# Kernel tuning notes

Measured on AMD Instinct MI355X. Metric: run time of the kernel, lower is better.

## Reference

```python
import jax, jax.numpy as jnp
import numpy as np

B, D, E = 8192, 2048, 8


def setup_inputs() -> dict:
    key = jax.random.key(0)
    k1, k2, k3, k4 = jax.random.split(key, 4)
    x = jax.random.normal(k1, (B, D), dtype=jnp.float32)
    W = jax.random.normal(k2, (E, D, D), dtype=jnp.float32) * (1.0 / np.sqrt(D))
    b = jax.random.normal(k3, (E, D), dtype=jnp.float32) * 0.02
    module_indices = jax.random.randint(k4, (B,), 0, E, dtype=jnp.int64)
    return {"x": x, "W": W, "b": b, "module_indices": module_indices}


def reference(x, W, b, module_indices):
    # Each row i of x is processed by expert module_indices[i]:
    #   out[i] = x[i] @ W[e] + b[e],  e = module_indices[i]
    # Vectorized as: run every expert on every token (E dense GEMMs),
    # then select the assigned expert per token via one-hot combine.
    y_all = jnp.einsum('bd,edo->beo', x, W) + b[None, :, :]   # [B, E, D]
    onehot = jax.nn.one_hot(module_indices, W.shape[0], dtype=x.dtype)  # [B, E]
    out = jnp.einsum('beo,be->bo', y_all, onehot)             # [B, D]
    return out
```

## Files before the change

### kernel.cpp

```cpp
#include <hip/hip_runtime.h>
#include <hip/hip_bf16.h>
#include <stdint.h>


#define B_TOK 8192
#define DIM   2048
#define NEXP  8
#define BM 128
#define BN 128
#define BK 32

typedef __attribute__((ext_vector_type(4))) float f32x4;
typedef __attribute__((ext_vector_type(8))) short s16x8;

__device__ __forceinline__ uint32_t f2bf(float f) {
    uint32_t u = __float_as_uint(f);
    uint32_t r = u + 0x7fffu + ((u >> 16) & 1u);
    return r >> 16;
}

__device__ __forceinline__ void async16(const void* g, void* l) {
    __builtin_amdgcn_global_load_lds(
        (const __attribute__((address_space(1))) uint32_t*)g,
        (__attribute__((address_space(3))) uint32_t*)l, 16, 0, 0);
}

__global__ __launch_bounds__(256) void k_route(const int* __restrict__ idx,
                                               int* __restrict__ meta,
                                               int* __restrict__ perm) {
    __shared__ int cnt[256][9];
    __shared__ int offS[NEXP + 1];
    int t = threadIdx.x;
    int myIdx[32];
    #pragma unroll
    for (int i = 0; i < 32; ++i) myIdx[i] = idx[t * 32 + i];
    int c[NEXP] = {0, 0, 0, 0, 0, 0, 0, 0};
    #pragma unroll
    for (int i = 0; i < 32; ++i) {
        int e = myIdx[i];
        #pragma unroll
        for (int k = 0; k < NEXP; ++k) c[k] += (e == k) ? 1 : 0;
    }
    #pragma unroll
    for (int k = 0; k < NEXP; ++k) cnt[t][k] = c[k];
    __syncthreads();
    if (t < NEXP) {
        int run = 0;
        for (int j = 0; j < 256; ++j) { int v = cnt[j][t]; cnt[j][t] = run; run += v; }
        offS[t] = run;
    }
    __syncthreads();
    if (t == 0) {
        int off = 0;
        #pragma unroll
        for (int e = 0; e < NEXP; ++e) {
            int v = offS[e];
            offS[e] = off; meta[16 + e] = off; off += v;
        }
        offS[NEXP] = off; meta[16 + NEXP] = off;
    }
    __syncthreads();
    int base[NEXP];
    #pragma unroll
    for (int k = 0; k < NEXP; ++k) base[k] = offS[k] + cnt[t][k];
    #pragma unroll
    for (int i = 0; i < 32; ++i) {
        int e = myIdx[i];
        int pos = 0;
        #pragma unroll
        for (int k = 0; k < NEXP; ++k) pos += (e == k) ? base[k] : 0;
        perm[pos] = t * 32 + i;
        #pragma unroll
        for (int k = 0; k < NEXP; ++k) base[k] += (e == k) ? 1 : 0;
    }
}

__global__ __launch_bounds__(256) void k_gather(const float* __restrict__ x,
                                                const int* __restrict__ perm,
                                                uint16_t* __restrict__ xs) {
    int p = blockIdx.x;
    int src = perm[p];
    int t = threadIdx.x;
    const float4* xin = (const float4*)(x + (size_t)src * DIM);
    float4 a = xin[2 * t];
    float4 c = xin[2 * t + 1];
    uint4 o;
    o.x = f2bf(a.x) | (f2bf(a.y) << 16);
    o.y = f2bf(a.z) | (f2bf(a.w) << 16);
    o.z = f2bf(c.x) | (f2bf(c.y) << 16);
    o.w = f2bf(c.z) | (f2bf(c.w) << 16);
    *(uint4*)(xs + (size_t)p * DIM + t * 8) = o;
}

__global__ __launch_bounds__(256) void k_wt(const float* __restrict__ W,
                                            uint16_t* __restrict__ Wt) {
    __shared__ uint32_t lds[64][65];
    int e = blockIdx.z, d0 = blockIdx.x * 128, o0 = blockIdx.y * 64;
    int t = threadIdx.x;
    const float* Wp = W + ((size_t)e * DIM + d0) * DIM + o0;
    #pragma unroll
    for (int p = 0; p < 4; ++p) {
        int dp = p * 16 + (t >> 4);
        int oc = (t & 15) * 4;
        const float* r0 = Wp + (size_t)(2 * dp) * DIM + oc;
        float4 v0 = *(const float4*)r0;
        float4 v1 = *(const float4*)(r0 + DIM);
        uint32_t w0 = f2bf(v0.x) | (f2bf(v1.x) << 16);
        uint32_t w1 = f2bf(v0.y) | (f2bf(v1.y) << 16);
        uint32_t w2 = f2bf(v0.z) | (f2bf(v1.z) << 16);
        uint32_t w3 = f2bf(v0.w) | (f2bf(v1.w) << 16);
        lds[oc + 0][dp ^ (((oc + 0) & 15) << 2)] = w0;
        lds[oc + 1][dp ^ (((oc + 1) & 15) << 2)] = w1;
        lds[oc + 2][dp ^ (((oc + 2) & 15) << 2)] = w2;
        lds[oc + 3][dp ^ (((oc + 3) & 15) << 2)] = w3;
    }
    __syncthreads();
    uint16_t* Wo = Wt + ((size_t)e * DIM + o0) * DIM + d0;
    #pragma unroll
    for (int q = 0; q < 4; ++q) {
        int o = q * 16 + (t >> 4);
        int cb = ((t & 15) * 4) ^ ((o & 15) << 2);
        uint4 w = *(const uint4*)&lds[o][cb];
        *(uint4*)(Wo + (size_t)o * DIM + (t & 15) * 8) = w;
    }
}

__global__ __launch_bounds__(256) void k_gemm(
    const uint16_t* __restrict__ xs, const uint16_t* __restrict__ Wt,
    const float* __restrict__ bias, const int* __restrict__ meta,
    const int* __restrict__ perm, float* __restrict__ out) {
    __shared__ uint16_t As[BM * BK];
    __shared__ uint16_t Bs[BN * BK];
    __shared__ int permS[BM];

    int id = blockIdx.y;
    int e = -1, seg0 = 0, segc = 0;
    for (int i = 0; i < NEXP; ++i) {
        int o0 = meta[16 + i], o1 = meta[16 + i + 1];
        int tiles = (o1 - o0 + BM - 1) / BM;
        if (id < tiles) { e = i; seg0 = o0; segc = o1 - o0; break; }
        id -= tiles;
    }
    if (e < 0) return;
    int m0 = seg0 + id * BM;
    int valid = segc - id * BM; if (valid > BM) valid = BM;
    int n0 = blockIdx.x * BN;

    int tid = threadIdx.x;
    if (tid < BM) permS[tid] = (tid < valid) ? perm[m0 + tid] : 0;

    int wave = tid >> 6, lane = tid & 63;
    int wm = (wave >> 1) * 64, wn = (wave & 1) * 64;
    int lr = lane & 15, quad = lane >> 4;

    f32x4 acc[4][4] = {};

    const uint16_t* aG = xs + (size_t)m0 * DIM;
    const uint16_t* bG = Wt + ((size_t)e * DIM + n0) * DIM;

    for (int k0 = 0; k0 < DIM; k0 += BK) {
        #pragma unroll
        for (int ro = 0; ro < 2; ++ro) {
            int ch = ro * 256 + tid;
            int row = ch >> 2, kc = (ch & 3) * 8;
            async16(aG + (size_t)row * DIM + k0 + kc, As + ch * 8);
            async16(bG + (size_t)row * DIM + k0 + kc, Bs + ch * 8);
        }
        __syncthreads();

        s16x8 af[4], bf[4];
        #pragma unroll
        for (int i = 0; i < 4; ++i)
            af[i] = *(const s16x8*)(As + (wm + i * 16 + lr) * BK + quad * 8);
        #pragma unroll
        for (int i = 0; i < 4; ++i)
            bf[i] = *(const s16x8*)(Bs + (wn + i * 16 + lr) * BK + quad * 8);
        #pragma unroll
        for (int i = 0; i < 4; ++i)
            #pragma unroll
            for (int j = 0; j < 4; ++j)
                acc[i][j] = __builtin_amdgcn_mfma_f32_16x16x32_bf16(af[i], bf[j], acc[i][j], 0, 0, 0);
        __syncthreads();
    }

    #pragma unroll
    for (int j = 0; j < 4; ++j) {
        int col = n0 + wn + j * 16 + lr;
        float bv = bias[e * DIM + col];
        #pragma unroll
        for (int i = 0; i < 4; ++i) {
            #pragma unroll
            for (int r = 0; r < 4; ++r) {
                int lrow = wm + i * 16 + quad * 4 + r;
                if (lrow < valid) {
                    out[(size_t)permS[lrow] * DIM + col] = acc[i][j][r] + bv;
                }
            }
        }
    }
}

extern "C" void kernel_launch(void* const* d_in, const int* in_sizes, int n_in,
                              void* d_out, int out_size, void* d_ws, size_t ws_size,
                              hipStream_t stream) {
    const float* x    = (const float*)d_in[0];
    const float* W    = (const float*)d_in[1];
    const float* bias = (const float*)d_in[2];
    const int*   idx  = (const int*)d_in[3];
    float* out = (float*)d_out;

    char* ws = (char*)d_ws;
    int* meta = (int*)ws;
    int* perm = (int*)(ws + 256);
    uint16_t* xs = (uint16_t*)(ws + 65536);
    uint16_t* Wt = (uint16_t*)(ws + 65536 + (size_t)(B_TOK + BM) * DIM * 2);

    k_route<<<1, 256, 0, stream>>>(idx, meta, perm);
    k_gather<<<B_TOK, 256, 0, stream>>>(x, perm, xs);
    k_wt<<<dim3(DIM / 128, DIM / 64, NEXP), 256, 0, stream>>>(W, Wt);
    k_gemm<<<dim3(DIM / BN, B_TOK / BM + NEXP, 1), 256, 0, stream>>>(
        xs, Wt, bias, meta, perm, out);
}
```

Before: 412.5 us.

## Enlarge GEMM tiles, double-buffer swizzled LDS, fuse prep kernels and gather

Merges routing, x-to-bf16 conversion and W transpose into a single prep launch, and moves the token gather into the GEMM's load addressing via perm. The GEMM uses 256x256x64 tiles with 512 threads, double-buffered LDS staging with prefetch of the next k-slice, and an XOR swizzle on LDS columns. It aims to cut launch overhead, global traffic per FLOP and bank conflicts. In exchange it raises LDS use to about 128KB per block, limiting occupancy, and wastes more work on partial expert tiles.

```diff
diff --git a/kernel.cpp b/kernel.cpp
--- a/kernel.cpp
+++ b/kernel.cpp
@@ -6,9 +6,9 @@
 #define B_TOK 8192
 #define DIM   2048
 #define NEXP  8
-#define BM 128
-#define BN 128
-#define BK 32
+#define BM 256
+#define BN 256
+#define BK 64
 
 typedef __attribute__((ext_vector_type(4))) float f32x4;
 typedef __attribute__((ext_vector_type(8))) short s16x8;
@@ -25,78 +25,83 @@
         (__attribute__((address_space(3))) uint32_t*)l, 16, 0, 0);
 }
 
-__global__ __launch_bounds__(256) void k_route(const int* __restrict__ idx,
-                                               int* __restrict__ meta,
-                                               int* __restrict__ perm) {
-    __shared__ int cnt[256][9];
-    __shared__ int offS[NEXP + 1];
+__global__ __launch_bounds__(256) void k_prep(const float* __restrict__ x,
+                                              const float* __restrict__ W,
+                                              const int* __restrict__ idx,
+                                              int* __restrict__ meta,
+                                              int* __restrict__ perm,
+                                              uint16_t* __restrict__ xb,
+                                              uint16_t* __restrict__ Wt) {
+    __shared__ __align__(16) char smem[16640];
+    int bid = blockIdx.x;
     int t = threadIdx.x;
-    int myIdx[32];
-    #pragma unroll
-    for (int i = 0; i < 32; ++i) myIdx[i] = idx[t * 32 + i];
-    int c[NEXP] = {0, 0, 0, 0, 0, 0, 0, 0};
-    #pragma unroll
-    for (int i = 0; i < 32; ++i) {
-        int e = myIdx[i];
-        #pragma unroll
-        for (int k = 0; k < NEXP; ++k) c[k] += (e == k) ? 1 : 0;
-    }
-    #pragma unroll
-    for (int k = 0; k < NEXP; ++k) cnt[t][k] = c[k];
-    __syncthreads();
-    if (t < NEXP) {
-        int run = 0;
-        for (int j = 0; j < 256; ++j) { int v = cnt[j][t]; cnt[j][t] = run; run += v; }
-        offS[t] = run;
-    }
-    __syncthreads();
-    if (t == 0) {
-        int off = 0;
-        #pragma unroll
-        for (int e = 0; e < NEXP; ++e) {
-            int v = offS[e];
-            offS[e] = off; meta[16 + e] = off; off += v;
-        }
-        offS[NEXP] = off; meta[16 + NEXP] = off;
-    }
-    __syncthreads();
-    int base[NEXP];
-    #pragma unroll
-    for (int k = 0; k < NEXP; ++k) base[k] = offS[k] + cnt[t][k];
-    #pragma unroll
-    for (int i = 0; i < 32; ++i) {
-        int e = myIdx[i];
-        int pos = 0;
-        #pragma unroll
-        for (int k = 0; k < NEXP; ++k) pos += (e == k) ? base[k] : 0;
-        perm[pos] = t * 32 + i;
-        #pragma unroll
-        for (int k = 0; k < NEXP; ++k) base[k] += (e == k) ? 1 : 0;
-    }
-}
-
-__global__ __launch_bounds__(256) void k_gather(const float* __restrict__ x,
-                                                const int* __restrict__ perm,
-                                                uint16_t* __restrict__ xs) {
-    int p = blockIdx.x;
-    int src = perm[p];
-    int t = threadIdx.x;
-    const float4* xin = (const float4*)(x + (size_t)src * DIM);
-    float4 a = xin[2 * t];
-    float4 c = xin[2 * t + 1];
-    uint4 o;
-    o.x = f2bf(a.x) | (f2bf(a.y) << 16);
-    o.y = f2bf(a.z) | (f2bf(a.w) << 16);
-    o.z = f2bf(c.x) | (f2bf(c.y) << 16);
-    o.w = f2bf(c.z) | (f2bf(c.w) << 16);
-    *(uint4*)(xs + (size_t)p * DIM + t * 8) = o;
-}
-
-__global__ __launch_bounds__(256) void k_wt(const float* __restrict__ W,
-                                            uint16_t* __restrict__ Wt) {
-    __shared__ uint32_t lds[64][65];
-    int e = blockIdx.z, d0 = blockIdx.x * 128, o0 = blockIdx.y * 64;
-    int t = threadIdx.x;
+
+    if (bid == 0) {
+        int (*cnt)[9] = (int(*)[9])smem;
+        int* offS = (int*)(smem + 9216);
+        int myIdx[32];
+        #pragma unroll
+        for (int i = 0; i < 32; ++i) myIdx[i] = idx[t * 32 + i];
+        int c[NEXP] = {0, 0, 0, 0, 0, 0, 0, 0};
+        #pragma unroll
+        for (int i = 0; i < 32; ++i) {
+            int e = myIdx[i];
+            #pragma unroll
+            for (int k = 0; k < NEXP; ++k) c[k] += (e == k) ? 1 : 0;
+        }
+        #pragma unroll
+        for (int k = 0; k < NEXP; ++k) cnt[t][k] = c[k];
+        __syncthreads();
+        if (t < NEXP) {
+            int run = 0;
+            for (int j = 0; j < 256; ++j) { int v = cnt[j][t]; cnt[j][t] = run; run += v; }
+            offS[t] = run;
+        }
+        __syncthreads();
+        if (t == 0) {
+            int off = 0;
+            #pragma unroll
+            for (int e = 0; e < NEXP; ++e) {
+                int v = offS[e];
+                offS[e] = off; meta[16 + e] = off; off += v;
+            }
+            offS[NEXP] = off; meta[16 + NEXP] = off;
+        }
+        __syncthreads();
+        int base[NEXP];
+        #pragma unroll
+        for (int k = 0; k < NEXP; ++k) base[k] = offS[k] + cnt[t][k];
+        #pragma unroll
+        for (int i = 0; i < 32; ++i) {
+            int e = myIdx[i];
+            int pos = 0;
+            #pragma unroll
+            for (int k = 0; k < NEXP; ++k) pos += (e == k) ? base[k] : 0;
+            perm[pos] = t * 32 + i;
+            #pragma unroll
+            for (int k = 0; k < NEXP; ++k) base[k] += (e == k) ? 1 : 0;
+        }
+        return;
+    }
+
+    if (bid <= B_TOK) {
+        int p = bid - 1;
+        const float4* xin = (const float4*)(x + (size_t)p * DIM);
+        float4 a = xin[2 * t];
+        float4 c = xin[2 * t + 1];
+        uint4 o;
+        o.x = f2bf(a.x) | (f2bf(a.y) << 16);
+        o.y = f2bf(a.z) | (f2bf(a.w) << 16);
+        o.z = f2bf(c.x) | (f2bf(c.y) << 16);
+        o.w = f2bf(c.z) | (f2bf(c.w) << 16);
+        *(uint4*)(xb + (size_t)p * DIM + t * 8) = o;
+        return;
+    }
+
+    int wb = bid - (B_TOK + 1);
+    int bx = wb & 15, by = (wb >> 4) & 31, e = wb >> 9;
+    int d0 = bx * 128, o0 = by * 64;
+    uint32_t (*lds)[65] = (uint32_t(*)[65])smem;
     const float* Wp = W + ((size_t)e * DIM + d0) * DIM + o0;
     #pragma unroll
     for (int p = 0; p < 4; ++p) {
@@ -105,14 +110,10 @@
         const float* r0 = Wp + (size_t)(2 * dp) * DIM + oc;
         float4 v0 = *(const float4*)r0;
         float4 v1 = *(const float4*)(r0 + DIM);
-        uint32_t w0 = f2bf(v0.x) | (f2bf(v1.x) << 16);
-        uint32_t w1 = f2bf(v0.y) | (f2bf(v1.y) << 16);
-        uint32_t w2 = f2bf(v0.z) | (f2bf(v1.z) << 16);
-        uint32_t w3 = f2bf(v0.w) | (f2bf(v1.w) << 16);
-        lds[oc + 0][dp ^ (((oc + 0) & 15) << 2)] = w0;
-        lds[oc + 1][dp ^ (((oc + 1) & 15) << 2)] = w1;
-        lds[oc + 2][dp ^ (((oc + 2) & 15) << 2)] = w2;
-        lds[oc + 3][dp ^ (((oc + 3) & 15) << 2)] = w3;
+        lds[oc + 0][dp ^ (((oc + 0) & 15) << 2)] = f2bf(v0.x) | (f2bf(v1.x) << 16);
+        lds[oc + 1][dp ^ (((oc + 1) & 15) << 2)] = f2bf(v0.y) | (f2bf(v1.y) << 16);
+        lds[oc + 2][dp ^ (((oc + 2) & 15) << 2)] = f2bf(v0.z) | (f2bf(v1.z) << 16);
+        lds[oc + 3][dp ^ (((oc + 3) & 15) << 2)] = f2bf(v0.w) | (f2bf(v1.w) << 16);
     }
     __syncthreads();
     uint16_t* Wo = Wt + ((size_t)e * DIM + o0) * DIM + d0;
@@ -125,12 +126,12 @@
     }
 }
 
-__global__ __launch_bounds__(256) void k_gemm(
-    const uint16_t* __restrict__ xs, const uint16_t* __restrict__ Wt,
+__global__ __launch_bounds__(512, 2) void k_gemm(
+    const uint16_t* __restrict__ xb, const uint16_t* __restrict__ Wt,
     const float* __restrict__ bias, const int* __restrict__ meta,
     const int* __restrict__ perm, float* __restrict__ out) {
-    __shared__ uint16_t As[BM * BK];
-    __shared__ uint16_t Bs[BN * BK];
+    __shared__ uint16_t As[2][BM * BK];
+    __shared__ uint16_t Bs[2][BN * BK];
     __shared__ int permS[BM];
 
     int id = blockIdx.y;
@@ -150,37 +151,55 @@
     if (tid < BM) permS[tid] = (tid < valid) ? perm[m0 + tid] : 0;
 
     int wave = tid >> 6, lane = tid & 63;
-    int wm = (wave >> 1) * 64, wn = (wave & 1) * 64;
+    int wm = (wave >> 2) * 128, wn = (wave & 3) * 64;
     int lr = lane & 15, quad = lane >> 4;
 
-    f32x4 acc[4][4] = {};
-
-    const uint16_t* aG = xs + (size_t)m0 * DIM;
-    const uint16_t* bG = Wt + ((size_t)e * DIM + n0) * DIM;
-
+    const uint16_t* aSrc[4];
+    const uint16_t* bSrc[4];
+    #pragma unroll
+    for (int c = 0; c < 4; ++c) {
+        int ch = c * 512 + tid;
+        int row = ch >> 3;
+        int kc = ((ch & 7) ^ (row & 7)) * 8;
+        int pr = m0 + row; if (pr > B_TOK - 1) pr = B_TOK - 1;
+        aSrc[c] = xb + (size_t)perm[pr] * DIM + kc;
+        bSrc[c] = Wt + ((size_t)e * DIM + n0 + row) * DIM + kc;
+    }
+
+    auto STAGE = [&](int buf, int k0) {
+        #pragma unroll
+        for (int c = 0; c < 4; ++c) {
+            int ch = c * 512 + tid;
+            async16(aSrc[c] + k0, &As[buf][ch * 8]);
+            async16(bSrc[c] + k0, &Bs[buf][ch * 8]);
+        }
+    };
+
+    f32x4 acc[8][4] = {};
+    STAGE(0, 0);
+    __syncthreads();
+
+    int cur = 0;
+    int sw = lr & 7;
     for (int k0 = 0; k0 < DIM; k0 += BK) {
-        #pragma unroll
-        for (int ro = 0; ro < 2; ++ro) {
-            int ch = ro * 256 + tid;
-            int row = ch >> 2, kc = (ch & 3) * 8;
-            async16(aG + (size_t)row * DIM + k0 + kc, As + ch * 8);
-            async16(bG + (size_t)row * DIM + k0 + kc, Bs + ch * 8);
-        }
-        __syncthreads();
-
-        s16x8 af[4], bf[4];
-        #pragma unroll
-        for (int i = 0; i < 4; ++i)
-            af[i] = *(const s16x8*)(As + (wm + i * 16 + lr) * BK + quad * 8);
-        #pragma unroll
-        for (int i = 0; i < 4; ++i)
-            bf[i] = *(const s16x8*)(Bs + (wn + i * 16 + lr) * BK + quad * 8);
-        #pragma unroll
-        for (int i = 0; i < 4; ++i)
+        if (k0 + BK < DIM) STAGE(cur ^ 1, k0 + BK);
+        #pragma unroll
+        for (int s = 0; s < 2; ++s) {
+            s16x8 af[8], bfr[4];
+            #pragma unroll
+            for (int i = 0; i < 8; ++i)
+                af[i] = *(const s16x8*)&As[cur][(wm + i * 16 + lr) * BK + (((s * 4 + quad) ^ sw) * 8)];
             #pragma unroll
             for (int j = 0; j < 4; ++j)
-                acc[i][j] = __builtin_amdgcn_mfma_f32_16x16x32_bf16(af[i], bf[j], acc[i][j], 0, 0, 0);
-        __syncthreads();
+                bfr[j] = *(const s16x8*)&Bs[cur][(wn + j * 16 + lr) * BK + (((s * 4 + quad) ^ sw) * 8)];
+            #pragma unroll
+            for (int i = 0; i < 8; ++i)
+                #pragma unroll
+                for (int j = 0; j < 4; ++j)
+                    acc[i][j] = __builtin_amdgcn_mfma_f32_16x16x32_bf16(af[i], bfr[j], acc[i][j], 0, 0, 0);
+        }
+        __syncthreads();
+        cur ^= 1;
     }
 
     #pragma unroll
@@ -188,7 +207,7 @@
         int col = n0 + wn + j * 16 + lr;
         float bv = bias[e * DIM + col];
         #pragma unroll
-        for (int i = 0; i < 4; ++i) {
+        for (int i = 0; i < 8; ++i) {
             #pragma unroll
             for (int r = 0; r < 4; ++r) {
                 int lrow = wm + i * 16 + quad * 4 + r;
@@ -212,12 +231,10 @@
     char* ws = (char*)d_ws;
     int* meta = (int*)ws;
     int* perm = (int*)(ws + 256);
-    uint16_t* xs = (uint16_t*)(ws + 65536);
-    uint16_t* Wt = (uint16_t*)(ws + 65536 + (size_t)(B_TOK + BM) * DIM * 2);
-
-    k_route<<<1, 256, 0, stream>>>(idx, meta, perm);
-    k_gather<<<B_TOK, 256, 0, stream>>>(x, perm, xs);
-    k_wt<<<dim3(DIM / 128, DIM / 64, NEXP), 256, 0, stream>>>(W, Wt);
-    k_gemm<<<dim3(DIM / BN, B_TOK / BM + NEXP, 1), 256, 0, stream>>>(
-        xs, Wt, bias, meta, perm, out);
-}
+    uint16_t* xb = (uint16_t*)(ws + 65536);
+    uint16_t* Wt = (uint16_t*)(ws + 65536 + (size_t)B_TOK * DIM * 2);
+
+    k_prep<<<1 + B_TOK + 4096, 256, 0, stream>>>(x, W, idx, meta, perm, xb, Wt);
+    k_gemm<<<dim3(DIM / BN, B_TOK / BM + NEXP, 1), 512, 0, stream>>>(
+        xb, Wt, bias, meta, perm, out);
+}
```

Measured after the change: 436.3 us. +5.8%, slower.
